# Kernel tuning notes

Hardware: AMD Instinct MI355X
Metric: run time of the kernel (lower is better)

## Reference

```python
import jax, jax.numpy as jnp
import numpy as np

B, C, H, W = 32, 256, 56, 56
G, K, RR = 4, 7, 4
CR = C // RR


def setup_inputs() -> dict:
    key = jax.random.key(0)
    ks = jax.random.split(key, 10)
    s = jax.random.normal(ks[0], (B, C, H, W), jnp.float32)
    r = jax.random.normal(ks[1], (B, C, H, W), jnp.float32)
    b1 = 1.0 / np.sqrt(C)
    proj_w1 = jax.random.uniform(ks[2], (CR, C), jnp.float32, -b1, b1)
    proj_b1 = jax.random.uniform(ks[3], (CR,), jnp.float32, -b1, b1)
    b2 = 1.0 / np.sqrt(CR)
    proj_w2 = jax.random.uniform(ks[4], (C * G * 2, CR), jnp.float32, -b2, b2)
    proj_b2 = jax.random.uniform(ks[5], (C * G * 2,), jnp.float32, -b2, b2)
    # kaiming_uniform_(a=sqrt(5)) on [G, C, K, K]: fan_in = C*K*K, bound = sqrt(6/((1+5)*fan_in)) = 1/sqrt(fan_in)
    bw = 1.0 / np.sqrt(C * K * K)
    weight = jax.random.uniform(ks[6], (G, C, K, K), jnp.float32, -bw, bw)
    beta_scale = jnp.zeros((G, C), jnp.float32)  # original is [1,G,C,1,1] zeros
    bp = 1.0 / np.sqrt(C)
    pw_w = jax.random.uniform(ks[7], (C, C), jnp.float32, -bp, bp)
    pw_b = jax.random.uniform(ks[8], (C,), jnp.float32, -bp, bp)
    return {"s": s, "r": r, "proj_w1": proj_w1, "proj_b1": proj_b1,
            "proj_w2": proj_w2, "proj_b2": proj_b2, "weight": weight,
            "beta_scale": beta_scale, "pw_w": pw_w, "pw_b": pw_b}


def reference(s, r, proj_w1, proj_b1, proj_w2, proj_b2, weight, beta_scale, pw_w, pw_b):
    Bs, Cs, Hs, Ws = s.shape
    Gs, _, Ks, _ = weight.shape
    # squeeze-excite weight generation
    pooled = jnp.mean(r, axis=(2, 3))                                   # [B,C]
    h = jax.nn.gelu(pooled @ proj_w1.T + proj_b1, approximate=False)    # [B,C//rr]
    scale = (h @ proj_w2.T + proj_b2).reshape(Bs, Gs, Cs, 2)            # [B,G,C,2]
    alpha = jax.nn.softmax(scale[..., 0], axis=1)                       # softmax over groups
    beta = jnp.tanh(scale[..., 1] * jnp.exp(beta_scale)[None] * 0.1)    # [B,G,C]
    w = alpha[..., None, None] * weight[None] + beta[..., None, None]   # [B,G,C,K,K]
    # sum over groups == summing per-group depthwise conv outputs (conv linear in kernel)
    wk = jnp.sum(w, axis=1).reshape(Bs * Cs, 1, Ks, Ks)
    pad = Ks // 2
    out = jax.lax.conv_general_dilated(
        s.reshape(1, Bs * Cs, Hs, Ws), wk,
        window_strides=(1, 1), padding=[(pad, pad), (pad, pad)],
        dimension_numbers=("NCHW", "OIHW", "NCHW"),
        feature_group_count=Bs * Cs)                                     # [1,B*C,H,W]
    out = jax.nn.gelu(out, approximate=False).reshape(Bs, Cs, Hs, Ws)
    out = jnp.einsum("bchw,dc->bdhw", out, pw_w) + pw_b[None, :, None, None]
    return out
```

## Files before the change

### kernel.cpp

```cpp
#include <hip/hip_runtime.h>
#include <math.h>

typedef unsigned short u16;
typedef unsigned int   u32;
typedef __attribute__((ext_vector_type(8))) short  short8;
typedef __attribute__((ext_vector_type(4))) float  floatx4;

#define Bn  32
#define Cn  256
#define HWn 3136
#define Gn  4
#define CRn 64

__device__ __forceinline__ float gelu_f(float x) {
    return 0.5f * x * (1.0f + erff(x * 0.70710678118654752f));
}
__device__ __forceinline__ u16 f2bf(float f) {
    u32 u = __builtin_bit_cast(u32, f);
    u = (u + 0x7fffu + ((u >> 16) & 1u)) >> 16;
    return (u16)u;
}

__global__ __launch_bounds__(256) void k_pool(const float* __restrict__ r,
                                              const float* __restrict__ pw_w,
                                              float* __restrict__ pooled,
                                              u16* __restrict__ wbf) {
    int blk = blockIdx.x, t = threadIdx.x;
    if (blk >= Bn * Cn) {
        int base = (blk - Bn * Cn) * 1024 + t;
        #pragma unroll
        for (int i = 0; i < 4; i++) wbf[base + i * 256] = f2bf(pw_w[base + i * 256]);
        return;
    }
    const float4* src = (const float4*)(r + (size_t)blk * HWn);
    float sum = 0.f;
    for (int i = t; i < HWn / 4; i += 256) {
        float4 v = src[i];
        sum += (v.x + v.y) + (v.z + v.w);
    }
    #pragma unroll
    for (int off = 32; off >= 1; off >>= 1) sum += __shfl_down(sum, off, 64);
    __shared__ float red[4];
    if ((t & 63) == 0) red[t >> 6] = sum;
    __syncthreads();
    if (t == 0) pooled[blk] = (red[0] + red[1] + red[2] + red[3]) * (1.0f / 3136.0f);
}

__global__ __launch_bounds__(256) void k_wgen(const float* __restrict__ pooled,
                                              const float* __restrict__ w1,
                                              const float* __restrict__ b1,
                                              const float* __restrict__ w2,
                                              const float* __restrict__ b2,
                                              const float* __restrict__ weight,
                                              const float* __restrict__ beta_scale,
                                              float* __restrict__ wk) {
    int b = blockIdx.x, t = threadIdx.x;
    __shared__ float sp[Cn];
    __shared__ float sh[CRn];
    __shared__ float ssc[Cn * Gn * 2];
    sp[t] = pooled[b * Cn + t];
    __syncthreads();
    if (t < CRn) {
        float acc = b1[t];
        const float* wr = w1 + t * Cn;
        for (int c = 0; c < Cn; c++) acc += sp[c] * wr[c];
        sh[t] = gelu_f(acc);
    }
    __syncthreads();
    for (int i = t; i < Cn * Gn * 2; i += 256) {
        float acc = b2[i];
        const float* wr = w2 + i * CRn;
        #pragma unroll 8
        for (int j = 0; j < CRn; j++) acc += sh[j] * wr[j];
        ssc[i] = acc;
    }
    __syncthreads();
    float av[Gn], bt[Gn];
    float mx = -1e30f;
    #pragma unroll
    for (int g = 0; g < Gn; g++) {
        av[g] = ssc[(g * Cn + t) * 2 + 0];
        float s1 = ssc[(g * Cn + t) * 2 + 1];
        bt[g] = tanhf(s1 * expf(beta_scale[g * Cn + t]) * 0.1f);
        mx = fmaxf(mx, av[g]);
    }
    float se = 0.f;
    #pragma unroll
    for (int g = 0; g < Gn; g++) { av[g] = expf(av[g] - mx); se += av[g]; }
    float inv = 1.0f / se;
    #pragma unroll
    for (int g = 0; g < Gn; g++) av[g] *= inv;
    float bsum = bt[0] + bt[1] + bt[2] + bt[3];
    float* out = wk + ((size_t)b * Cn + t) * 49;
    for (int kk = 0; kk < 49; kk++) {
        float w = bsum;
        #pragma unroll
        for (int g = 0; g < Gn; g++) w += av[g] * weight[(g * Cn + t) * 49 + kk];
        out[kk] = w;
    }
}

__global__ __launch_bounds__(256) void k_dw(const float* __restrict__ s,
                                            const float* __restrict__ wk,
                                            u16* __restrict__ xdw) {
    int bc = blockIdx.x, t = threadIdx.x;
    __shared__ float kw[49];
    __shared__ float sin_[62 * 62];
    for (int i = t; i < 62 * 62; i += 256) sin_[i] = 0.f;
    if (t < 49) kw[t] = wk[(size_t)bc * 49 + t];
    __syncthreads();
    const float4* src = (const float4*)(s + (size_t)bc * HWn);
    for (int i = t; i < HWn / 4; i += 256) {
        float4 v = src[i];
        int row = i / 14;
        int col = (i % 14) * 4;
        float* dst = &sin_[(row + 3) * 62 + col + 3];
        dst[0] = v.x; dst[1] = v.y; dst[2] = v.z; dst[3] = v.w;
    }
    __syncthreads();
    if (t < 196) {
        int r0 = (t / 14) * 4, c0 = (t % 14) * 4;
        float acc[4][4] = {};
        #pragma unroll
        for (int a = 0; a < 10; a++) {
            float row10[10];
            const float* rp = &sin_[(r0 + a) * 62 + c0];
            #pragma unroll
            for (int x = 0; x < 10; x++) row10[x] = rp[x];
            #pragma unroll
            for (int i = 0; i < 4; i++) {
                int ky = a - i;
                if (ky >= 0 && ky < 7) {
                    #pragma unroll
                    for (int kx = 0; kx < 7; kx++) {
                        float wv = kw[ky * 7 + kx];
                        #pragma unroll
                        for (int j = 0; j < 4; j++) acc[i][j] += row10[j + kx] * wv;
                    }
                }
            }
        }
        u16* dst = xdw + (size_t)bc * HWn;
        #pragma unroll
        for (int i = 0; i < 4; i++) {
            u16 ov[4];
            #pragma unroll
            for (int j = 0; j < 4; j++) ov[j] = f2bf(gelu_f(acc[i][j]));
            *(uint2*)(dst + (r0 + i) * 56 + c0) = *(const uint2*)ov;
        }
    }
}

__global__ __launch_bounds__(256) void k_pw(const u16* __restrict__ xdw,
                                            const u16* __restrict__ wbf,
                                            const float* __restrict__ pw_b,
                                            float* __restrict__ out) {
    int tileHW = blockIdx.x;
    int tileD  = blockIdx.y;
    int b      = blockIdx.z;
    int t = threadIdx.x;
    int lane = t & 63;
    int wv = t >> 6;
    int waveM = wv >> 1, waveN = wv & 1;
    int hw0 = tileHW * 128;
    int d0  = tileD * 128;

    __shared__ __align__(16) u16 sA[128 * 40];
    __shared__ __align__(16) u16 sX[128 * 40];

    floatx4 acc[4][4];
    #pragma unroll
    for (int mi = 0; mi < 4; mi++)
        #pragma unroll
        for (int ni = 0; ni < 4; ni++) acc[mi][ni] = (floatx4){0.f, 0.f, 0.f, 0.f};

    int arow = t >> 2;
    int akc  = t & 3;
    int xc   = t >> 3;
    int xhc  = t & 7;
    int wgrp = (xc >> 3) ^ (xhc & 3);
    int scol = (wgrp << 3) | (xc & 7);

    const u16* Xbase = xdw + (size_t)b * Cn * HWn;
    int q = lane >> 4, l16 = lane & 15;

    for (int ks = 0; ks < 8; ks++) {
        int k0 = ks * 32;
        __syncthreads();
        #pragma unroll
        for (int half = 0; half < 2; half++) {
            int dd = arow + half * 64;
            short8 v = *(const short8*)(wbf + (d0 + dd) * 256 + k0 + akc * 8);
            *(short8*)(&sA[dd * 40 + akc * 8]) = v;
        }
        #pragma unroll
        for (int half = 0; half < 2; half++) {
            int colb = xhc * 8 + half * 64;
            int hw = hw0 + colb;
            short8 v = short8{0, 0, 0, 0, 0, 0, 0, 0};
            if (hw < HWn) v = *(const short8*)(Xbase + (size_t)(k0 + xc) * HWn + hw);
            const u16* vp = (const u16*)&v;
            #pragma unroll
            for (int e = 0; e < 8; e++) sX[(colb + e) * 40 + scol] = vp[e];
        }
        __syncthreads();
        short8 fa[4], fb[4];
        #pragma unroll
        for (int mi = 0; mi < 4; mi++) {
            int row = waveM * 64 + mi * 16 + l16;
            fa[mi] = *(const short8*)(&sA[row * 40 + q * 8]);
        }
        #pragma unroll
        for (int ni = 0; ni < 4; ni++) {
            int hwRow = waveN * 64 + ni * 16 + l16;
            int rgrp = q ^ ((hwRow >> 3) & 3);
            fb[ni] = *(const short8*)(&sX[hwRow * 40 + rgrp * 8]);
        }
        #pragma unroll
        for (int mi = 0; mi < 4; mi++)
            #pragma unroll
            for (int ni = 0; ni < 4; ni++)
                acc[mi][ni] = __builtin_amdgcn_mfma_f32_16x16x32_bf16(fa[mi], fb[ni], acc[mi][ni], 0, 0, 0);
    }
    #pragma unroll
    for (int mi = 0; mi < 4; mi++) {
        #pragma unroll
        for (int reg = 0; reg < 4; reg++) {
            int d = d0 + waveM * 64 + mi * 16 + q * 4 + reg;
            float bias = pw_b[d];
            #pragma unroll
            for (int ni = 0; ni < 4; ni++) {
                int hw = hw0 + waveN * 64 + ni * 16 + l16;
                if (hw < HWn)
                    out[((size_t)b * Cn + d) * HWn + hw] = acc[mi][ni][reg] + bias;
            }
        }
    }
}

extern "C" void kernel_launch(void* const* d_in, const int* in_sizes, int n_in,
                              void* d_out, int out_size, void* d_ws, size_t ws_size,
                              hipStream_t stream) {
    const float* s          = (const float*)d_in[0];
    const float* r          = (const float*)d_in[1];
    const float* proj_w1    = (const float*)d_in[2];
    const float* proj_b1    = (const float*)d_in[3];
    const float* proj_w2    = (const float*)d_in[4];
    const float* proj_b2    = (const float*)d_in[5];
    const float* weight     = (const float*)d_in[6];
    const float* beta_scale = (const float*)d_in[7];
    const float* pw_w       = (const float*)d_in[8];
    const float* pw_b       = (const float*)d_in[9];
    float* out = (float*)d_out;

    char* ws = (char*)d_ws;
    float* pooled = (float*)(ws);
    u16*   wbf    = (u16*)(ws + 32768);
    float* wk     = (float*)(ws + 163840);
    u16*   xdw    = (u16*)(ws + 2097152);

    k_pool<<<Bn * Cn + 64, 256, 0, stream>>>(r, pw_w, pooled, wbf);
    k_wgen<<<Bn, 256, 0, stream>>>(pooled, proj_w1, proj_b1, proj_w2, proj_b2,
                                   weight, beta_scale, wk);
    k_dw<<<Bn * Cn, 256, 0, stream>>>(s, wk, xdw);
    k_pw<<<dim3(25, 2, Bn), 256, 0, stream>>>(xdw, wbf, pw_b, out);
}
```

Measured before the change: 401.1 us.

## Retile depthwise and pointwise kernels, use fast erf approximation for GELU

```diff
diff --git a/kernel.cpp b/kernel.cpp
--- a/kernel.cpp
+++ b/kernel.cpp
@@ -14,6 +14,16 @@
 
 __device__ __forceinline__ float gelu_f(float x) {
     return 0.5f * x * (1.0f + erff(x * 0.70710678118654752f));
+}
+__device__ __forceinline__ float gelu_fast(float x) {
+    float ax = fabsf(x);
+    float y  = ax * 0.70710678118654752f;
+    float t  = __builtin_amdgcn_rcpf(fmaf(0.3275911f, y, 1.0f));
+    float p  = fmaf(fmaf(fmaf(fmaf(1.061405429f, t, -1.453152027f), t,
+                              1.421413741f), t, -0.284496736f), t, 0.254829592f) * t;
+    float e  = __builtin_amdgcn_exp2f(-y * y * 1.442695040888963f);
+    float er = fmaf(-p, e, 1.0f);
+    return fmaf(0.5f * ax, er, 0.5f * x);
 }
 __device__ __forceinline__ u16 f2bf(float f) {
     u32 u = __builtin_bit_cast(u32, f);
@@ -100,17 +110,21 @@
     }
 }
 
-__global__ __launch_bounds__(256) void k_dw(const float* __restrict__ s,
+__global__ __launch_bounds__(128) void k_dw(const float* __restrict__ s,
                                             const float* __restrict__ wk,
                                             u16* __restrict__ xdw) {
     int bc = blockIdx.x, t = threadIdx.x;
     __shared__ float kw[49];
     __shared__ float sin_[62 * 62];
-    for (int i = t; i < 62 * 62; i += 256) sin_[i] = 0.f;
+    {
+        float4 z = {0.f, 0.f, 0.f, 0.f};
+        float4* p = (float4*)sin_;
+        for (int i = t; i < 961; i += 128) p[i] = z;
+    }
     if (t < 49) kw[t] = wk[(size_t)bc * 49 + t];
     __syncthreads();
     const float4* src = (const float4*)(s + (size_t)bc * HWn);
-    for (int i = t; i < HWn / 4; i += 256) {
+    for (int i = t; i < HWn / 4; i += 128) {
         float4 v = src[i];
         int row = i / 14;
         int col = (i % 14) * 4;
@@ -118,17 +132,17 @@
         dst[0] = v.x; dst[1] = v.y; dst[2] = v.z; dst[3] = v.w;
     }
     __syncthreads();
-    if (t < 196) {
-        int r0 = (t / 14) * 4, c0 = (t % 14) * 4;
-        float acc[4][4] = {};
-        #pragma unroll
-        for (int a = 0; a < 10; a++) {
+    if (t < 112) {
+        int r0 = (t / 14) * 7, c0 = (t % 14) * 4;
+        float acc[7][4] = {};
+        #pragma unroll
+        for (int a = 0; a < 13; a++) {
             float row10[10];
             const float* rp = &sin_[(r0 + a) * 62 + c0];
             #pragma unroll
             for (int x = 0; x < 10; x++) row10[x] = rp[x];
             #pragma unroll
-            for (int i = 0; i < 4; i++) {
+            for (int i = 0; i < 7; i++) {
                 int ky = a - i;
                 if (ky >= 0 && ky < 7) {
                     #pragma unroll
@@ -142,10 +156,10 @@
         }
         u16* dst = xdw + (size_t)bc * HWn;
         #pragma unroll
-        for (int i = 0; i < 4; i++) {
+        for (int i = 0; i < 7; i++) {
             u16 ov[4];
             #pragma unroll
-            for (int j = 0; j < 4; j++) ov[j] = f2bf(gelu_f(acc[i][j]));
+            for (int j = 0; j < 4; j++) ov[j] = f2bf(gelu_fast(acc[i][j]));
             *(uint2*)(dst + (r0 + i) * 56 + c0) = *(const uint2*)ov;
         }
     }
@@ -156,17 +170,14 @@
                                             const float* __restrict__ pw_b,
                                             float* __restrict__ out) {
     int tileHW = blockIdx.x;
-    int tileD  = blockIdx.y;
-    int b      = blockIdx.z;
+    int b      = blockIdx.y;
     int t = threadIdx.x;
     int lane = t & 63;
     int wv = t >> 6;
-    int waveM = wv >> 1, waveN = wv & 1;
-    int hw0 = tileHW * 128;
-    int d0  = tileD * 128;
-
-    __shared__ __align__(16) u16 sA[128 * 40];
-    __shared__ __align__(16) u16 sX[128 * 40];
+    int hw0 = tileHW * 64;
+
+    __shared__ __align__(16) u16 sA[256 * 40];
+    __shared__ __align__(16) u16 sX[64 * 40];
 
     floatx4 acc[4][4];
     #pragma unroll
@@ -188,31 +199,27 @@
         int k0 = ks * 32;
         __syncthreads();
         #pragma unroll
-        for (int half = 0; half < 2; half++) {
-            int dd = arow + half * 64;
-            short8 v = *(const short8*)(wbf + (d0 + dd) * 256 + k0 + akc * 8);
+        for (int quarter = 0; quarter < 4; quarter++) {
+            int dd = arow + quarter * 64;
+            short8 v = *(const short8*)(wbf + dd * 256 + k0 + akc * 8);
             *(short8*)(&sA[dd * 40 + akc * 8]) = v;
         }
-        #pragma unroll
-        for (int half = 0; half < 2; half++) {
-            int colb = xhc * 8 + half * 64;
-            int hw = hw0 + colb;
-            short8 v = short8{0, 0, 0, 0, 0, 0, 0, 0};
-            if (hw < HWn) v = *(const short8*)(Xbase + (size_t)(k0 + xc) * HWn + hw);
+        {
+            short8 v = *(const short8*)(Xbase + (size_t)(k0 + xc) * HWn + hw0 + xhc * 8);
             const u16* vp = (const u16*)&v;
             #pragma unroll
-            for (int e = 0; e < 8; e++) sX[(colb + e) * 40 + scol] = vp[e];
+            for (int e = 0; e < 8; e++) sX[(xhc * 8 + e) * 40 + scol] = vp[e];
         }
         __syncthreads();
         short8 fa[4], fb[4];
         #pragma unroll
         for (int mi = 0; mi < 4; mi++) {
-            int row = waveM * 64 + mi * 16 + l16;
+            int row = wv * 64 + mi * 16 + l16;
             fa[mi] = *(const short8*)(&sA[row * 40 + q * 8]);
         }
         #pragma unroll
         for (int ni = 0; ni < 4; ni++) {
-            int hwRow = waveN * 64 + ni * 16 + l16;
+            int hwRow = ni * 16 + l16;
             int rgrp = q ^ ((hwRow >> 3) & 3);
             fb[ni] = *(const short8*)(&sX[hwRow * 40 + rgrp * 8]);
         }
@@ -226,13 +233,12 @@
     for (int mi = 0; mi < 4; mi++) {
         #pragma unroll
         for (int reg = 0; reg < 4; reg++) {
-            int d = d0 + waveM * 64 + mi * 16 + q * 4 + reg;
+            int d = wv * 64 + mi * 16 + q * 4 + reg;
             float bias = pw_b[d];
             #pragma unroll
             for (int ni = 0; ni < 4; ni++) {
-                int hw = hw0 + waveN * 64 + ni * 16 + l16;
-                if (hw < HWn)
-                    out[((size_t)b * Cn + d) * HWn + hw] = acc[mi][ni][reg] + bias;
+                int hw = hw0 + ni * 16 + l16;
+                out[((size_t)b * Cn + d) * HWn + hw] = acc[mi][ni][reg] + bias;
             }
         }
     }
@@ -262,6 +268,6 @@
     k_pool<<<Bn * Cn + 64, 256, 0, stream>>>(r, pw_w, pooled, wbf);
     k_wgen<<<Bn, 256, 0, stream>>>(pooled, proj_w1, proj_b1, proj_w2, proj_b2,
                                    weight, beta_scale, wk);
-    k_dw<<<Bn * Cn, 256, 0, stream>>>(s, wk, xdw);
-    k_pw<<<dim3(25, 2, Bn), 256, 0, stream>>>(xdw, wbf, pw_b, out);
-}
+    k_dw<<<Bn * Cn, 128, 0, stream>>>(s, wk, xdw);
+    k_pw<<<dim3(49, Bn), 256, 0, stream>>>(xdw, wbf, pw_b, out);
+}
```

Result: faster. 365.4 us (-8.9%).
